# Performance work log

Measured on AMD Instinct MI355X. Metric: run time of the kernel, lower is better.

## Reference

```python
import jax, jax.numpy as jnp
import numpy as np

NEG_INF = -jnp.inf


def setup_inputs() -> dict:
    B, V = 128, 128000
    key = jax.random.key(0)
    k1, k2, k3, k4, k5 = jax.random.split(key, 5)
    logits = jax.random.normal(k1, (B, V), dtype=jnp.float32)
    # temperatures in [0.1, 1.0) to avoid divide-by-tiny blowups
    temperatures = jax.random.uniform(k2, (B,), dtype=jnp.float32) * 0.9 + 0.1
    # min_p typically small, in [0, 0.1)
    min_ps = jax.random.uniform(k3, (B,), dtype=jnp.float32) * 0.1
    # top_p in [0.1, 1.0)
    top_ps = jax.random.uniform(k4, (B,), dtype=jnp.float32) * 0.9 + 0.1
    # top_k in [1, 1000)
    top_ks = jax.random.randint(k5, (B,), 1, 1000, dtype=jnp.int32)
    return {"logits": logits, "temperatures": temperatures, "min_ps": min_ps,
            "top_ps": top_ps, "top_ks": top_ks}


def _apply_top_k_top_p(logits, top_ps, top_ks):
    B, V = logits.shape
    sort_idx = jnp.argsort(logits, axis=-1)  # ascending, matches torch sort(descending=False)
    logits_sort = jnp.take_along_axis(logits, sort_idx, axis=-1)
    # top-k: threshold is the (V-k)-th smallest value; mask anything strictly below it
    thresh_idx = (V - top_ks.astype(jnp.int32))[:, None]          # [B,1]
    thresh = jnp.take_along_axis(logits_sort, thresh_idx, axis=-1)  # [B,1]
    logits_sort = jnp.where(logits_sort < thresh, NEG_INF, logits_sort)
    # top-p: drop smallest tokens whose cumulative prob <= 1 - p; never drop the max token
    probs_sort = jax.nn.softmax(logits_sort, axis=-1)
    probs_sum = jnp.cumsum(probs_sort, axis=-1)
    top_p_mask = probs_sum <= (1.0 - top_ps)[:, None]
    top_p_mask = top_p_mask.at[:, -1].set(False)
    logits_sort = jnp.where(top_p_mask, NEG_INF, logits_sort)
    # scatter back to original vocab order
    rows = jnp.arange(B)[:, None]
    return jnp.zeros_like(logits_sort).at[rows, sort_idx].set(logits_sort)


def _apply_min_p(logits, min_ps):
    probs = jax.nn.softmax(logits, axis=-1)
    top_probs = jnp.max(probs, axis=-1, keepdims=True)
    remove = probs < min_ps[:, None] * top_probs
    return jnp.where(remove, NEG_INF, logits)


def reference(logits, temperatures, min_ps, top_ps, top_ks):
    logits = logits.astype(jnp.float32) / temperatures[:, None]
    logits = _apply_top_k_top_p(logits, top_ps, top_ks)
    logits = _apply_min_p(logits, min_ps)
    # torch.multinomial(softmax(logits), 1) == categorical sampling from logits
    sample_key = jax.random.key(42)
    next_tokens = jax.random.categorical(sample_key, logits, axis=-1)  # [B]
    return next_tokens
```

## Files before the change

### kernel.cpp

```cpp
#include <hip/hip_runtime.h>
#include <stdint.h>

#define HBINS 4096
#define CAND 2048
#define NSLICES 32
#define HTHREADS 256
#define CTHREADS 256
#define STHREADS 1024

typedef unsigned int u32;
typedef unsigned long long u64;

__device__ __forceinline__ u32 f2s(float f) {
  u32 b = __float_as_uint(f);
  return b ^ ((b & 0x80000000u) ? 0xFFFFFFFFu : 0x80000000u);
}
__device__ __forceinline__ float s2f(u32 s) {
  u32 b = (s & 0x80000000u) ? (s ^ 0x80000000u) : ~s;
  return __uint_as_float(b);
}
__device__ __forceinline__ u32 rotl32(u32 x, int r) { return (x << r) | (x >> (32 - r)); }

__device__ __forceinline__ u64 shfl_xor_u64(u64 v, int mask) {
  int lo = __shfl_xor((int)(u32)v, mask, 64);
  int hi = __shfl_xor((int)(u32)(v >> 32), mask, 64);
  return ((u64)(u32)hi << 32) | (u32)lo;
}

__device__ __forceinline__ u32 threefry_bits(u32 ctr) {
  const u32 ks0 = 0u, ks1 = 42u, ks2 = 0x1BD11BDAu ^ 0u ^ 42u;
  u32 x0 = ks0;
  u32 x1 = ctr + ks1;
#define TFR(r) { x0 += x1; x1 = rotl32(x1, (r)); x1 ^= x0; }
  TFR(13) TFR(15) TFR(26) TFR(6)   x0 += ks1; x1 += ks2 + 1u;
  TFR(17) TFR(29) TFR(16) TFR(24)  x0 += ks2; x1 += ks0 + 2u;
  TFR(13) TFR(15) TFR(26) TFR(6)   x0 += ks0; x1 += ks1 + 3u;
  TFR(17) TFR(29) TFR(16) TFR(24)  x0 += ks1; x1 += ks2 + 4u;
  TFR(13) TFR(15) TFR(26) TFR(6)   x0 += ks2; x1 += ks0 + 5u;
#undef TFR
  return x0 ^ x1;
}

__global__ __launch_bounds__(HTHREADS)
void hist_kernel(const float* __restrict__ logits, u32* __restrict__ ghist,
                 int V, int slice_len) {
  const int row = blockIdx.x / NSLICES;
  const int sl  = blockIdx.x % NSLICES;
  const int tid = threadIdx.x;
  __shared__ u32 h[HBINS];
  for (int i = tid; i < HBINS; i += HTHREADS) h[i] = 0u;
  __syncthreads();
  int rem = V - sl * slice_len;
  if (rem > slice_len) rem = slice_len;
  if (rem < 0) rem = 0;
  const float* src = logits + (size_t)row * (size_t)V + (size_t)sl * slice_len;
  const int n4 = rem >> 2;
  const float4* p4 = (const float4*)src;
  for (int i = tid; i < n4; i += HTHREADS) {
    float4 w = p4[i];
    atomicAdd(&h[f2s(w.x) >> 20], 1u);
    atomicAdd(&h[f2s(w.y) >> 20], 1u);
    atomicAdd(&h[f2s(w.z) >> 20], 1u);
    atomicAdd(&h[f2s(w.w) >> 20], 1u);
  }
  for (int i = (n4 << 2) + tid; i < rem; i += HTHREADS)
    atomicAdd(&h[f2s(src[i]) >> 20], 1u);
  __syncthreads();
  u32* gh = ghist + (size_t)row * HBINS;
  for (int i = tid; i < HBINS; i += HTHREADS) {
    u32 c = h[i];
    if (c) atomicAdd(&gh[i], c);
  }
}

__global__ __launch_bounds__(256)
void select_kernel(const u32* __restrict__ ghist, const int* __restrict__ topks,
                   u32* __restrict__ gthr, u32* __restrict__ gcs,
                   u32* __restrict__ gcount, int V) {
  const int row = blockIdx.x;
  const int tid = threadIdx.x;
  __shared__ u32 hist[HBINS];
  __shared__ u32 part[256];
  __shared__ u32 chunk[64];
  const u32* gh = ghist + (size_t)row * HBINS;
  for (int i = tid; i < HBINS; i += 256) hist[i] = gh[i];
  __syncthreads();
  {
    u32 s = 0;
    for (int j = 0; j < 16; ++j) s += hist[tid * 16 + j];
    part[tid] = s;
  }
  __syncthreads();
  if (tid < 64)
    chunk[tid] = part[tid * 4] + part[tid * 4 + 1] + part[tid * 4 + 2] + part[tid * 4 + 3];
  __syncthreads();
  if (tid == 0) {
    int k = topks[row];
    if (k < 1) k = 1;
    if (k > V) k = V;
    const u32 ku = (u32)k;
    u32 acc = 0;
    int cstar = 0;
    for (int c = 63; c >= 0; --c) {
      if (acc + chunk[c] >= ku) { cstar = c; break; }
      acc += chunk[c];
    }
    int pstar = cstar * 4;
    for (int p = cstar * 4 + 3; p >= cstar * 4; --p) {
      if (acc + part[p] >= ku) { pstar = p; break; }
      acc += part[p];
    }
    int bstar = pstar * 16;
    for (int bq = pstar * 16 + 15; bq >= pstar * 16; --bq) {
      acc += hist[bq];
      if (acc >= ku) { bstar = bq; break; }
    }
    gthr[row] = (u32)bstar << 20;
    gcs[row] = (acc < (u32)CAND ? acc : (u32)CAND);
    gcount[row] = 0u;
  }
}

__global__ __launch_bounds__(CTHREADS)
void collect_kernel(const float* __restrict__ logits,
                    const float* __restrict__ temps,
                    const u32* __restrict__ gthr,
                    u32* __restrict__ gcount,
                    u64* __restrict__ gcand, int V, int slice_len) {
  const int row = blockIdx.x / NSLICES;
  const int sl  = blockIdx.x % NSLICES;
  const int tid = threadIdx.x;

  __shared__ u64 stage[CAND];
  __shared__ int sh_cnt, sh_base;
  if (tid == 0) sh_cnt = 0;
  __syncthreads();

  const u32 thr = gthr[row];
  const float t = temps[row];
  int rem = V - sl * slice_len;
  if (rem > slice_len) rem = slice_len;
  if (rem < 0) rem = 0;
  const float* src = logits + (size_t)row * (size_t)V + (size_t)sl * slice_len;
  const u32 ibase = (u32)(sl * slice_len);
  const int n4 = rem >> 2;
  const float4* p4 = (const float4*)src;
  for (int i = tid; i < n4; i += CTHREADS) {
    float4 w = p4[i];
    if (f2s(w.x) >= thr) { int pos = atomicAdd(&sh_cnt, 1); if (pos < CAND) stage[pos] = ((u64)f2s(w.x / t) << 32) | (ibase + 4u * i + 0u); }
    if (f2s(w.y) >= thr) { int pos = atomicAdd(&sh_cnt, 1); if (pos < CAND) stage[pos] = ((u64)f2s(w.y / t) << 32) | (ibase + 4u * i + 1u); }
    if (f2s(w.z) >= thr) { int pos = atomicAdd(&sh_cnt, 1); if (pos < CAND) stage[pos] = ((u64)f2s(w.z / t) << 32) | (ibase + 4u * i + 2u); }
    if (f2s(w.w) >= thr) { int pos = atomicAdd(&sh_cnt, 1); if (pos < CAND) stage[pos] = ((u64)f2s(w.w / t) << 32) | (ibase + 4u * i + 3u); }
  }
  for (int i = (n4 << 2) + tid; i < rem; i += CTHREADS) {
    float l = src[i];
    if (f2s(l) >= thr) { int pos = atomicAdd(&sh_cnt, 1); if (pos < CAND) stage[pos] = ((u64)f2s(l / t) << 32) | (ibase + (u32)i); }
  }
  __syncthreads();
  int n = sh_cnt;
  if (n > CAND) n = CAND;
  if (tid == 0) sh_base = (int)atomicAdd(&gcount[row], (u32)n);
  __syncthreads();
  const int base = sh_base;
  u64* gc = gcand + (size_t)row * CAND;
  for (int i = tid; i < n; i += CTHREADS) {
    int dst = base + i;
    if (dst < CAND) gc[dst] = stage[i];
  }
}

__global__ __launch_bounds__(STHREADS)
void Sampler_73529840107542_kernel(const float* __restrict__ minps,
                                   const float* __restrict__ topps,
                                   const int* __restrict__ topks,
                                   const u32* __restrict__ gcs,
                                   const u64* __restrict__ gcand,
                                   int* __restrict__ out, int V) {
  const int b = blockIdx.x;
  const int tid = threadIdx.x;
  const int w = tid >> 6, l = tid & 63;
  const float one_minus_p = 1.0f - topps[b];
  const float minp = minps[b];
  int k = topks[b];
  if (k < 1) k = 1;
  if (k > V) k = V;

  __shared__ u64 cand[CAND];
  __shared__ u64 scand[CAND];
  __shared__ float eBuf[CAND];
  __shared__ float bufA[CAND];
  __shared__ float bufB[CAND];
  __shared__ unsigned char keepf[CAND];
  __shared__ u32 rbin[256];
  __shared__ float wredf[16];
  __shared__ u64 wred64[16];
  __shared__ int sh_byte, sh_above, sh_ns;
  __shared__ float sh_Z1, sh_Z2;

  const int cs = (int)gcs[b];
  const u64* gc = gcand + (size_t)b * CAND;
  for (int c = tid; c < cs; c += STHREADS) cand[c] = gc[c];
  if (tid == 0) sh_ns = 0;
  __syncthreads();

  u32 prefix = 0u;
  u32 remk = (u32)k;
  for (int pass = 0; pass < 4; ++pass) {
    const int shift = 24 - 8 * pass;
    if (tid < 256) rbin[tid] = 0u;
    __syncthreads();
    const u32 mask = (pass == 0) ? 0u : (0xFFFFFFFFu << (shift + 8));
    for (int c = tid; c < cs; c += STHREADS) {
      u32 s = (u32)(cand[c] >> 32);
      if (((s ^ prefix) & mask) == 0u)
        atomicAdd(&rbin[(s >> shift) & 255u], 1u);
    }
    __syncthreads();
    if (w == 0) {
      u32 b0 = rbin[4 * l], b1 = rbin[4 * l + 1], b2 = rbin[4 * l + 2], b3 = rbin[4 * l + 3];
      u32 q3 = b3, q2 = b2 + q3, q1 = b1 + q2, q0 = b0 + q1;
      u32 inc = q0;
      #pragma unroll
      for (int off = 1; off < 64; off <<= 1) {
        int src = l + off;
        u32 o = (u32)__shfl((int)inc, src < 64 ? src : l, 64);
        inc += (src < 64) ? o : 0u;
      }
      u32 excl = inc - q0;
      u64 ball = __ballot(excl + q0 >= remk);
      int lsel = 63 - __clzll(ball);
      if (l == lsel) {
        int i; u32 above;
        if      (excl + q3 >= remk) { i = 3; above = excl; }
        else if (excl + q2 >= remk) { i = 2; above = excl + q3; }
        else if (excl + q1 >= remk) { i = 1; above = excl + q2; }
        else                        { i = 0; above = excl + q1; }
        sh_byte = 4 * l + i;
        sh_above = (int)above;
      }
    }
    __syncthreads();
    prefix |= ((u32)sh_byte) << shift;
    remk -= (u32)sh_above;
  }
  const u32 Ts = prefix;

  for (int c = tid; c < cs; c += STHREADS) {
    u64 key = cand[c];
    if ((u32)(key >> 32) >= Ts) {
      int pos = atomicAdd(&sh_ns, 1);
      scand[pos] = key;
    }
  }
  __syncthreads();
  const int ns = sh_ns;

  int SN = 128;
  while (SN < ns) SN <<= 1;
  const int NW = SN >> 7;
  const bool act = (w < NW);
  const int e_lo = (w << 7) + l;
  const int e_hi = e_lo + 64;
  const u64 SENT = 0xFFFFFFFFFFFFFFFFull;
  u64 k0 = (act && e_lo < ns) ? scand[e_lo] : SENT;
  u64 k1 = (act && e_hi < ns) ? scand[e_hi] : SENT;
  for (int size = 2; size <= SN; size <<= 1) {
    for (int s = size >> 1; s > 0; s >>= 1) {
      if (s >= 128) {
        if (act) { scand[e_lo] = k0; scand[e_hi] = k1; }
        __syncthreads();
        if (act) {
          u64 p0 = scand[e_lo ^ s], p1 = scand[e_hi ^ s];
          bool km0 = (((e_lo & s) == 0) == ((e_lo & size) == 0));
          if (km0 ? (p0 < k0) : (p0 > k0)) k0 = p0;
          bool km1 = (((e_hi & s) == 0) == ((e_hi & size) == 0));
          if (km1 ? (p1 < k1) : (p1 > k1)) k1 = p1;
        }
        __syncthreads();
      } else if (act) {
        if (s == 64) {
          bool asc = ((e_lo & size) == 0);
          if ((k0 > k1) == asc) { u64 t = k0; k0 = k1; k1 = t; }
        } else {
          u64 p0 = shfl_xor_u64(k0, s);
          u64 p1 = shfl_xor_u64(k1, s);
          bool km0 = (((l & s) == 0) == ((e_lo & size) == 0));
          if (km0 ? (p0 < k0) : (p0 > k0)) k0 = p0;
          bool km1 = (((l & s) == 0) == ((e_hi & size) == 0));
          if (km1 ? (p1 < k1) : (p1 > k1)) k1 = p1;
        }
      }
    }
  }
  if (act) { scand[e_lo] = k0; scand[e_hi] = k1; }
  __syncthreads();

  const float m = s2f((u32)(scand[ns - 1] >> 32));

  for (int c = tid; c < ns; c += STHREADS)
    eBuf[c] = expf(s2f((u32)(scand[c] >> 32)) - m);
  __syncthreads();

  {
    float local = 0.0f;
    for (int c = tid; c < ns; c += STHREADS) local += eBuf[c];
    #pragma unroll
    for (int off = 1; off < 64; off <<= 1) local += __shfl_xor(local, off, 64);
    if (l == 0) wredf[w] = local;
    __syncthreads();
    if (w == 0) {
      float v = (l < 16) ? wredf[l] : 0.0f;
      #pragma unroll
      for (int off = 1; off < 64; off <<= 1) v += __shfl_xor(v, off, 64);
      if (l == 0) sh_Z1 = v;
    }
    __syncthreads();
  }

  const float Z1 = sh_Z1;
  for (int c = tid; c < ns; c += STHREADS) bufA[c] = eBuf[c] / Z1;
  __syncthreads();

  if (w == 0) {
    float carry = 0.0f;
    for (int base = 0; base < ns; base += 64) {
      int c = base + l;
      float v = (c < ns) ? bufA[c] : 0.0f;
      float acc = carry;
      #pragma unroll 16
      for (int j = 0; j < 64; ++j) {
        float t = __shfl(v, j, 64);
        acc += (l >= j) ? t : 0.0f;
      }
      if (c < ns) bufB[c] = acc;
      carry = __shfl(acc, 63, 64);
    }
  }
  __syncthreads();

  for (int c = tid; c < ns; c += STHREADS)
    keepf[c] = (c == ns - 1 || bufB[c] > one_minus_p) ? 1 : 0;
  __syncthreads();

  {
    float local = 0.0f;
    for (int c = tid; c < ns; c += STHREADS)
      if (keepf[c]) local += eBuf[c];
    #pragma unroll
    for (int off = 1; off < 64; off <<= 1) local += __shfl_xor(local, off, 64);
    if (l == 0) wredf[w] = local;
    __syncthreads();
    if (w == 0) {
      float v = (l < 16) ? wredf[l] : 0.0f;
      #pragma unroll
      for (int off = 1; off < 64; off <<= 1) v += __shfl_xor(v, off, 64);
      if (l == 0) sh_Z2 = v;
    }
    __syncthreads();
  }

  {
    const float Z2 = sh_Z2;
    const float rhs = minp * (1.0f / Z2);
    for (int c = tid; c < ns; c += STHREADS)
      if (keepf[c] && (eBuf[c] / Z2 < rhs)) keepf[c] = 0;
  }
  __syncthreads();

  {
    const float TINY = 1.17549435082228750797e-38f;
    u64 best = 0ull;
    for (int c = tid; c < ns; c += STHREADS) {
      if (!keepf[c]) continue;
      u32 s = (u32)(scand[c] >> 32);
      u32 idx = (u32)(scand[c] & 0xFFFFFFFFull);
      float x = s2f(s);
      u32 bits = threefry_bits((u32)b * (u32)V + idx);
      float f = __uint_as_float((bits >> 9) | 0x3f800000u) - 1.0f;
      float u = fmaxf(TINY, f * 1.0f + TINY);
      float g = -logf(-logf(u));
      float sc = g + x;
      u64 key = ((u64)f2s(sc) << 32) | (u64)(0xFFFFFFFFu - idx);
      if (key > best) best = key;
    }
    #pragma unroll
    for (int off = 1; off < 64; off <<= 1) {
      u64 o = shfl_xor_u64(best, off);
      if (o > best) best = o;
    }
    if (l == 0) wred64[w] = best;
    __syncthreads();
    if (w == 0) {
      u64 v = (l < 16) ? wred64[l] : 0ull;
      #pragma unroll
      for (int off = 1; off < 64; off <<= 1) {
        u64 o = shfl_xor_u64(v, off);
        if (o > v) v = o;
      }
      if (l == 0) out[b] = (int)(0xFFFFFFFFu - (u32)(v & 0xFFFFFFFFull));
    }
  }
}

extern "C" void kernel_launch(void* const* d_in, const int* in_sizes, int n_in,
                              void* d_out, int out_size, void* d_ws, size_t ws_size,
                              hipStream_t stream) {
  const float* logits = (const float*)d_in[0];
  const float* temps  = (const float*)d_in[1];
  const float* minps  = (const float*)d_in[2];
  const float* topps  = (const float*)d_in[3];
  const int*   topks  = (const int*)d_in[4];
  const int B = in_sizes[1];
  const int V = in_sizes[0] / B;
  (void)n_in; (void)out_size; (void)ws_size;

  u32* ghist  = (u32*)d_ws;
  u32* gcount = ghist + (size_t)B * HBINS;
  u32* gcs    = gcount + B;
  u32* gthr   = gcs + B;
  u64* gcand  = (u64*)(gthr + B);

  const int slice_len = (((V + NSLICES - 1) / NSLICES) + 3) & ~3;

  hipMemsetAsync(ghist, 0, (size_t)B * HBINS * sizeof(u32), stream);
  hist_kernel<<<dim3(B * NSLICES), dim3(HTHREADS), 0, stream>>>(logits, ghist, V, slice_len);
  select_kernel<<<dim3(B), dim3(256), 0, stream>>>(ghist, topks, gthr, gcs, gcount, V);
  collect_kernel<<<dim3(B * NSLICES), dim3(CTHREADS), 0, stream>>>(
      logits, temps, gthr, gcount, gcand, V, slice_len);
  Sampler_73529840107542_kernel<<<dim3(B), dim3(STHREADS), 0, stream>>>(
      minps, topps, topks, gcs, gcand, (int*)d_out, V);
}
```

Measured before the change: 179.0 us.

## Rewrite sampler as single-wavefront kernel with register bitonic sort

The final sampler kernel drops from 1024 threads to one 64-lane wavefront. Block barriers become block fences, the radix histogram gets four privatized copies to cut atomic contention, and compaction uses ballot/popcount instead of shared atomics. Candidate sets of up to 1024 are sorted in registers with shuffle-based bitonic stages. The histogram pass also gets its own slice count (16) separate from the collect pass, so it launches fewer, larger blocks. The cost is far less parallelism per row in the sampler, and a slow LDS fallback sort when there are more than 1024 candidates.

```diff
diff --git a/kernel.cpp b/kernel.cpp
--- a/kernel.cpp
+++ b/kernel.cpp
@@ -3,10 +3,10 @@
 
 #define HBINS 4096
 #define CAND 2048
-#define NSLICES 32
+#define HSLICES 16
+#define CSLICES 32
 #define HTHREADS 256
 #define CTHREADS 256
-#define STHREADS 1024
 
 typedef unsigned int u32;
 typedef unsigned long long u64;
@@ -41,11 +41,39 @@
   return x0 ^ x1;
 }
 
+template<int SIZE>
+__device__ __forceinline__ void shfl_sweep(u64* keys, int nr, int l) {
+  for (int s = (SIZE / 2 < 32 ? SIZE / 2 : 32); s >= 1; s >>= 1) {
+#pragma unroll
+    for (int r = 0; r < 16; ++r) {
+      if (r < nr) {
+        u64 pk = shfl_xor_u64(keys[r], s);
+        bool asc = ((((r << 6) + l) & SIZE) == 0);
+        bool keepmin = (((l & s) == 0) == asc);
+        if (keepmin ? (pk < keys[r]) : (pk > keys[r])) keys[r] = pk;
+      }
+    }
+  }
+}
+template<int SIZE, int D>
+__device__ __forceinline__ void local_phase(u64* keys, int nr) {
+#pragma unroll
+  for (int r = 0; r < 16; ++r) {
+    if (((r & D) == 0) && ((r | D) < 16)) {
+      if ((r | D) < nr) {
+        bool asc = (((r << 6) & SIZE) == 0);
+        u64 a = keys[r], b2 = keys[r | D];
+        if ((a > b2) == asc) { keys[r] = b2; keys[r | D] = a; }
+      }
+    }
+  }
+}
+
 __global__ __launch_bounds__(HTHREADS)
 void hist_kernel(const float* __restrict__ logits, u32* __restrict__ ghist,
                  int V, int slice_len) {
-  const int row = blockIdx.x / NSLICES;
-  const int sl  = blockIdx.x % NSLICES;
+  const int row = blockIdx.x / HSLICES;
+  const int sl  = blockIdx.x % HSLICES;
   const int tid = threadIdx.x;
   __shared__ u32 h[HBINS];
   for (int i = tid; i < HBINS; i += HTHREADS) h[i] = 0u;
@@ -127,8 +155,8 @@
                     const u32* __restrict__ gthr,
                     u32* __restrict__ gcount,
                     u64* __restrict__ gcand, int V, int slice_len) {
-  const int row = blockIdx.x / NSLICES;
-  const int sl  = blockIdx.x % NSLICES;
+  const int row = blockIdx.x / CSLICES;
+  const int sl  = blockIdx.x % CSLICES;
   const int tid = threadIdx.x;
 
   __shared__ u64 stage[CAND];
@@ -169,7 +197,7 @@
   }
 }
 
-__global__ __launch_bounds__(STHREADS)
+__global__ __launch_bounds__(64)
 void Sampler_73529840107542_kernel(const float* __restrict__ minps,
                                    const float* __restrict__ topps,
                                    const int* __restrict__ topks,
@@ -177,201 +205,172 @@
                                    const u64* __restrict__ gcand,
                                    int* __restrict__ out, int V) {
   const int b = blockIdx.x;
-  const int tid = threadIdx.x;
-  const int w = tid >> 6, l = tid & 63;
+  const int l = threadIdx.x;
   const float one_minus_p = 1.0f - topps[b];
   const float minp = minps[b];
   int k = topks[b];
   if (k < 1) k = 1;
   if (k > V) k = V;
 
-  __shared__ u64 cand[CAND];
-  __shared__ u64 scand[CAND];
-  __shared__ float eBuf[CAND];
-  __shared__ float bufA[CAND];
-  __shared__ float bufB[CAND];
-  __shared__ unsigned char keepf[CAND];
-  __shared__ u32 rbin[256];
-  __shared__ float wredf[16];
-  __shared__ u64 wred64[16];
-  __shared__ int sh_byte, sh_above, sh_ns;
-  __shared__ float sh_Z1, sh_Z2;
+  __shared__ __align__(16) unsigned char arena[36864];
+  u64* ldsCand = (u64*)(arena);
+  float* eArr  = (float*)(arena);
+  unsigned char* keep = arena + 8192;
+  u64* scand   = (u64*)(arena + 16384);
+  u32* rbin    = (u32*)(arena + 32768);
 
   const int cs = (int)gcs[b];
   const u64* gc = gcand + (size_t)b * CAND;
-  for (int c = tid; c < cs; c += STHREADS) cand[c] = gc[c];
-  if (tid == 0) sh_ns = 0;
-  __syncthreads();
+  for (int c = l; c < cs; c += 64) ldsCand[c] = gc[c];
+  __threadfence_block();
 
   u32 prefix = 0u;
   u32 remk = (u32)k;
   for (int pass = 0; pass < 4; ++pass) {
     const int shift = 24 - 8 * pass;
-    if (tid < 256) rbin[tid] = 0u;
-    __syncthreads();
+    for (int i = l; i < 1024; i += 64) rbin[i] = 0u;
+    __threadfence_block();
     const u32 mask = (pass == 0) ? 0u : (0xFFFFFFFFu << (shift + 8));
-    for (int c = tid; c < cs; c += STHREADS) {
-      u32 s = (u32)(cand[c] >> 32);
+    for (int c = l; c < cs; c += 64) {
+      u32 s = (u32)(ldsCand[c] >> 32);
       if (((s ^ prefix) & mask) == 0u)
-        atomicAdd(&rbin[(s >> shift) & 255u], 1u);
-    }
-    __syncthreads();
-    if (w == 0) {
-      u32 b0 = rbin[4 * l], b1 = rbin[4 * l + 1], b2 = rbin[4 * l + 2], b3 = rbin[4 * l + 3];
-      u32 q3 = b3, q2 = b2 + q3, q1 = b1 + q2, q0 = b0 + q1;
-      u32 inc = q0;
-      #pragma unroll
-      for (int off = 1; off < 64; off <<= 1) {
-        int src = l + off;
-        u32 o = (u32)__shfl((int)inc, src < 64 ? src : l, 64);
-        inc += (src < 64) ? o : 0u;
+        atomicAdd(&rbin[((l & 3) << 8) + ((s >> shift) & 255u)], 1u);
+    }
+    __threadfence_block();
+    u32 b0 = rbin[4 * l]     + rbin[256 + 4 * l]     + rbin[512 + 4 * l]     + rbin[768 + 4 * l];
+    u32 b1 = rbin[4 * l + 1] + rbin[256 + 4 * l + 1] + rbin[512 + 4 * l + 1] + rbin[768 + 4 * l + 1];
+    u32 b2 = rbin[4 * l + 2] + rbin[256 + 4 * l + 2] + rbin[512 + 4 * l + 2] + rbin[768 + 4 * l + 2];
+    u32 b3 = rbin[4 * l + 3] + rbin[256 + 4 * l + 3] + rbin[512 + 4 * l + 3] + rbin[768 + 4 * l + 3];
+    u32 q3 = b3, q2 = b2 + q3, q1 = b1 + q2, q0 = b0 + q1;
+    u32 inc = q0;
+#pragma unroll
+    for (int off = 1; off < 64; off <<= 1) {
+      int src = l + off;
+      u32 o = (u32)__shfl((int)inc, src < 64 ? src : l, 64);
+      inc += (src < 64) ? o : 0u;
+    }
+    u32 excl = inc - q0;
+    u64 ball = __ballot(excl + q0 >= remk);
+    int lsel = 63 - __clzll(ball);
+    int ii; u32 above;
+    if      (excl + q3 >= remk) { ii = 3; above = excl; }
+    else if (excl + q2 >= remk) { ii = 2; above = excl + q3; }
+    else if (excl + q1 >= remk) { ii = 1; above = excl + q2; }
+    else                        { ii = 0; above = excl + q1; }
+    u32 mybyte = (u32)(4 * l + ii);
+    u32 selbyte = (u32)__shfl((int)mybyte, lsel, 64);
+    u32 selabove = (u32)__shfl((int)above, lsel, 64);
+    prefix |= selbyte << shift;
+    remk -= selabove;
+  }
+  const u32 Ts = prefix;
+
+  int ns = 0;
+  for (int base2 = 0; base2 < cs; base2 += 64) {
+    int c = base2 + l;
+    u64 key = 0ull;
+    bool pred = false;
+    if (c < cs) {
+      key = ldsCand[c];
+      pred = ((u32)(key >> 32) >= Ts);
+    }
+    u64 ball = __ballot(pred);
+    if (pred) scand[ns + (int)__popcll(ball & ((1ull << l) - 1ull))] = key;
+    ns += (int)__popcll(ball);
+  }
+  __threadfence_block();
+
+  const u64 SENT = 0xFFFFFFFFFFFFFFFFull;
+  if (ns <= 1024) {
+    int SN = 64;
+    while (SN < ns) SN <<= 1;
+    const int nr = SN >> 6;
+    u64 keys[16];
+#pragma unroll
+    for (int r = 0; r < 16; ++r) {
+      if (r < nr) {
+        int e = (r << 6) + l;
+        keys[r] = (e < ns) ? scand[e] : SENT;
       }
-      u32 excl = inc - q0;
-      u64 ball = __ballot(excl + q0 >= remk);
-      int lsel = 63 - __clzll(ball);
-      if (l == lsel) {
-        int i; u32 above;
-        if      (excl + q3 >= remk) { i = 3; above = excl; }
-        else if (excl + q2 >= remk) { i = 2; above = excl + q3; }
-        else if (excl + q1 >= remk) { i = 1; above = excl + q2; }
-        else                        { i = 0; above = excl + q1; }
-        sh_byte = 4 * l + i;
-        sh_above = (int)above;
+    }
+    if (SN >= 2)  shfl_sweep<2>(keys, nr, l);
+    if (SN >= 4)  shfl_sweep<4>(keys, nr, l);
+    if (SN >= 8)  shfl_sweep<8>(keys, nr, l);
+    if (SN >= 16) shfl_sweep<16>(keys, nr, l);
+    if (SN >= 32) shfl_sweep<32>(keys, nr, l);
+    if (SN >= 64) shfl_sweep<64>(keys, nr, l);
+    if (SN >= 128)  { local_phase<128, 1>(keys, nr); shfl_sweep<128>(keys, nr, l); }
+    if (SN >= 256)  { local_phase<256, 2>(keys, nr); local_phase<256, 1>(keys, nr); shfl_sweep<256>(keys, nr, l); }
+    if (SN >= 512)  { local_phase<512, 4>(keys, nr); local_phase<512, 2>(keys, nr); local_phase<512, 1>(keys, nr); shfl_sweep<512>(keys, nr, l); }
+    if (SN >= 1024) { local_phase<1024, 8>(keys, nr); local_phase<1024, 4>(keys, nr); local_phase<1024, 2>(keys, nr); local_phase<1024, 1>(keys, nr); shfl_sweep<1024>(keys, nr, l); }
+#pragma unroll
+    for (int r = 0; r < 16; ++r)
+      if (r < nr) scand[(r << 6) + l] = keys[r];
+  } else {
+    for (int c = ns + l; c < CAND; c += 64) scand[c] = SENT;
+    __threadfence_block();
+    for (int size = 2; size <= CAND; size <<= 1) {
+      for (int s = size >> 1; s > 0; s >>= 1) {
+        for (int i = l; i < CAND; i += 64) {
+          int j = i ^ s;
+          if (j > i) {
+            u64 a = scand[i], b2 = scand[j];
+            bool asc = ((i & size) == 0);
+            if ((a > b2) == asc) { scand[i] = b2; scand[j] = a; }
+          }
+        }
+        __threadfence_block();
       }
     }
-    __syncthreads();
-    prefix |= ((u32)sh_byte) << shift;
-    remk -= (u32)sh_above;
-  }
-  const u32 Ts = prefix;
-
-  for (int c = tid; c < cs; c += STHREADS) {
-    u64 key = cand[c];
-    if ((u32)(key >> 32) >= Ts) {
-      int pos = atomicAdd(&sh_ns, 1);
-      scand[pos] = key;
-    }
-  }
-  __syncthreads();
-  const int ns = sh_ns;
-
-  int SN = 128;
-  while (SN < ns) SN <<= 1;
-  const int NW = SN >> 7;
-  const bool act = (w < NW);
-  const int e_lo = (w << 7) + l;
-  const int e_hi = e_lo + 64;
-  const u64 SENT = 0xFFFFFFFFFFFFFFFFull;
-  u64 k0 = (act && e_lo < ns) ? scand[e_lo] : SENT;
-  u64 k1 = (act && e_hi < ns) ? scand[e_hi] : SENT;
-  for (int size = 2; size <= SN; size <<= 1) {
-    for (int s = size >> 1; s > 0; s >>= 1) {
-      if (s >= 128) {
-        if (act) { scand[e_lo] = k0; scand[e_hi] = k1; }
-        __syncthreads();
-        if (act) {
-          u64 p0 = scand[e_lo ^ s], p1 = scand[e_hi ^ s];
-          bool km0 = (((e_lo & s) == 0) == ((e_lo & size) == 0));
-          if (km0 ? (p0 < k0) : (p0 > k0)) k0 = p0;
-          bool km1 = (((e_hi & s) == 0) == ((e_hi & size) == 0));
-          if (km1 ? (p1 < k1) : (p1 > k1)) k1 = p1;
-        }
-        __syncthreads();
-      } else if (act) {
-        if (s == 64) {
-          bool asc = ((e_lo & size) == 0);
-          if ((k0 > k1) == asc) { u64 t = k0; k0 = k1; k1 = t; }
-        } else {
-          u64 p0 = shfl_xor_u64(k0, s);
-          u64 p1 = shfl_xor_u64(k1, s);
-          bool km0 = (((l & s) == 0) == ((e_lo & size) == 0));
-          if (km0 ? (p0 < k0) : (p0 > k0)) k0 = p0;
-          bool km1 = (((l & s) == 0) == ((e_hi & size) == 0));
-          if (km1 ? (p1 < k1) : (p1 > k1)) k1 = p1;
-        }
-      }
-    }
-  }
-  if (act) { scand[e_lo] = k0; scand[e_hi] = k1; }
-  __syncthreads();
+  }
+  __threadfence_block();
 
   const float m = s2f((u32)(scand[ns - 1] >> 32));
 
-  for (int c = tid; c < ns; c += STHREADS)
-    eBuf[c] = expf(s2f((u32)(scand[c] >> 32)) - m);
-  __syncthreads();
+  for (int c = l; c < ns; c += 64)
+    eArr[c] = expf(s2f((u32)(scand[c] >> 32)) - m);
+
+  float z1l = 0.0f;
+  for (int c = l; c < ns; c += 64) z1l += eArr[c];
+#pragma unroll
+  for (int off = 1; off < 64; off <<= 1) z1l += __shfl_xor(z1l, off, 64);
+  const float Z1 = z1l;
 
   {
-    float local = 0.0f;
-    for (int c = tid; c < ns; c += STHREADS) local += eBuf[c];
-    #pragma unroll
-    for (int off = 1; off < 64; off <<= 1) local += __shfl_xor(local, off, 64);
-    if (l == 0) wredf[w] = local;
-    __syncthreads();
-    if (w == 0) {
-      float v = (l < 16) ? wredf[l] : 0.0f;
-      #pragma unroll
-      for (int off = 1; off < 64; off <<= 1) v += __shfl_xor(v, off, 64);
-      if (l == 0) sh_Z1 = v;
-    }
-    __syncthreads();
-  }
-
-  const float Z1 = sh_Z1;
-  for (int c = tid; c < ns; c += STHREADS) bufA[c] = eBuf[c] / Z1;
-  __syncthreads();
-
-  if (w == 0) {
     float carry = 0.0f;
-    for (int base = 0; base < ns; base += 64) {
-      int c = base + l;
-      float v = (c < ns) ? bufA[c] : 0.0f;
+    for (int base2 = 0; base2 < ns; base2 += 64) {
+      int c = base2 + l;
+      float v = (c < ns) ? (eArr[c] / Z1) : 0.0f;
       float acc = carry;
-      #pragma unroll 16
+#pragma unroll 16
       for (int j = 0; j < 64; ++j) {
         float t = __shfl(v, j, 64);
         acc += (l >= j) ? t : 0.0f;
       }
-      if (c < ns) bufB[c] = acc;
+      if (c < ns)
+        keep[c] = (c == ns - 1 || acc > one_minus_p) ? 1 : 0;
       carry = __shfl(acc, 63, 64);
     }
   }
-  __syncthreads();
-
-  for (int c = tid; c < ns; c += STHREADS)
-    keepf[c] = (c == ns - 1 || bufB[c] > one_minus_p) ? 1 : 0;
-  __syncthreads();
+
+  float z2l = 0.0f;
+  for (int c = l; c < ns; c += 64)
+    if (keep[c]) z2l += eArr[c];
+#pragma unroll
+  for (int off = 1; off < 64; off <<= 1) z2l += __shfl_xor(z2l, off, 64);
+  const float Z2 = z2l;
 
   {
-    float local = 0.0f;
-    for (int c = tid; c < ns; c += STHREADS)
-      if (keepf[c]) local += eBuf[c];
-    #pragma unroll
-    for (int off = 1; off < 64; off <<= 1) local += __shfl_xor(local, off, 64);
-    if (l == 0) wredf[w] = local;
-    __syncthreads();
-    if (w == 0) {
-      float v = (l < 16) ? wredf[l] : 0.0f;
-      #pragma unroll
-      for (int off = 1; off < 64; off <<= 1) v += __shfl_xor(v, off, 64);
-      if (l == 0) sh_Z2 = v;
-    }
-    __syncthreads();
-  }
-
-  {
-    const float Z2 = sh_Z2;
     const float rhs = minp * (1.0f / Z2);
-    for (int c = tid; c < ns; c += STHREADS)
-      if (keepf[c] && (eBuf[c] / Z2 < rhs)) keepf[c] = 0;
-  }
-  __syncthreads();
+    for (int c = l; c < ns; c += 64)
+      if (keep[c] && (eArr[c] / Z2 < rhs)) keep[c] = 0;
+  }
 
   {
     const float TINY = 1.17549435082228750797e-38f;
     u64 best = 0ull;
-    for (int c = tid; c < ns; c += STHREADS) {
-      if (!keepf[c]) continue;
+    for (int c = l; c < ns; c += 64) {
+      if (!keep[c]) continue;
       u32 s = (u32)(scand[c] >> 32);
       u32 idx = (u32)(scand[c] & 0xFFFFFFFFull);
       float x = s2f(s);
@@ -383,22 +382,12 @@
       u64 key = ((u64)f2s(sc) << 32) | (u64)(0xFFFFFFFFu - idx);
       if (key > best) best = key;
     }
-    #pragma unroll
+#pragma unroll
     for (int off = 1; off < 64; off <<= 1) {
       u64 o = shfl_xor_u64(best, off);
       if (o > best) best = o;
     }
-    if (l == 0) wred64[w] = best;
-    __syncthreads();
-    if (w == 0) {
-      u64 v = (l < 16) ? wred64[l] : 0ull;
-      #pragma unroll
-      for (int off = 1; off < 64; off <<= 1) {
-        u64 o = shfl_xor_u64(v, off);
-        if (o > v) v = o;
-      }
-      if (l == 0) out[b] = (int)(0xFFFFFFFFu - (u32)(v & 0xFFFFFFFFull));
-    }
+    if (l == 0) out[b] = (int)(0xFFFFFFFFu - (u32)(best & 0xFFFFFFFFull));
   }
 }
 
@@ -420,13 +409,14 @@
   u32* gthr   = gcs + B;
   u64* gcand  = (u64*)(gthr + B);
 
-  const int slice_len = (((V + NSLICES - 1) / NSLICES) + 3) & ~3;
+  const int hslice = (((V + HSLICES - 1) / HSLICES) + 3) & ~3;
+  const int cslice = (((V + CSLICES - 1) / CSLICES) + 3) & ~3;
 
   hipMemsetAsync(ghist, 0, (size_t)B * HBINS * sizeof(u32), stream);
-  hist_kernel<<<dim3(B * NSLICES), dim3(HTHREADS), 0, stream>>>(logits, ghist, V, slice_len);
+  hist_kernel<<<dim3(B * HSLICES), dim3(HTHREADS), 0, stream>>>(logits, ghist, V, hslice);
   select_kernel<<<dim3(B), dim3(256), 0, stream>>>(ghist, topks, gthr, gcs, gcount, V);
-  collect_kernel<<<dim3(B * NSLICES), dim3(CTHREADS), 0, stream>>>(
-      logits, temps, gthr, gcount, gcand, V, slice_len);
-  Sampler_73529840107542_kernel<<<dim3(B), dim3(STHREADS), 0, stream>>>(
+  collect_kernel<<<dim3(B * CSLICES), dim3(CTHREADS), 0, stream>>>(
+      logits, temps, gthr, gcount, gcand, V, cslice);
+  Sampler_73529840107542_kernel<<<dim3(B), dim3(64), 0, stream>>>(
       minps, topps, topks, gcs, gcand, (int*)d_out, V);
 }
```

Measured after the change: 256.1 us. +43.1%, slower.

## Fuse histogram, threshold select and candidate collection into one per-slice kernel

Applied to the files above, without the earlier changes.

Replaces the global histogram, per-row select kernel and collect kernel with a single kernel in which each slice builds a local histogram, picks a local threshold keeping roughly its top 128 values, and writes those candidates. This removes the large ghist memset, two launches and one of the two passes over the logits from global memory. The sampler also switches to warp-aggregated ballot atomics for its radix histogram, merges several shared buffers into one arena, and fuses the cumsum with the keep-flag step. The risk is correctness for top_k near 1000: 16 slices times 128 local candidates gives only about 2048 per row, so a slice holding many true top-k values could drop some of them.

```diff
diff --git a/kernel.cpp b/kernel.cpp
--- a/kernel.cpp
+++ b/kernel.cpp
@@ -2,11 +2,13 @@
 #include <stdint.h>
 
 #define HBINS 4096
-#define CAND 2048
-#define NSLICES 32
-#define HTHREADS 256
+#define CAND 4096
+#define SCAP 2048
+#define CSLICES 16
 #define CTHREADS 256
 #define STHREADS 1024
+#define TLOC 128
+#define STAGECAP 1024
 
 typedef unsigned int u32;
 typedef unsigned long long u64;
@@ -41,50 +43,42 @@
   return x0 ^ x1;
 }
 
-__global__ __launch_bounds__(HTHREADS)
-void hist_kernel(const float* __restrict__ logits, u32* __restrict__ ghist,
-                 int V, int slice_len) {
-  const int row = blockIdx.x / NSLICES;
-  const int sl  = blockIdx.x % NSLICES;
+__global__ __launch_bounds__(CTHREADS)
+void collect2_kernel(const float* __restrict__ logits,
+                     const float* __restrict__ temps,
+                     u32* __restrict__ gcount,
+                     u64* __restrict__ gcand, int V, int slice_len) {
+  const int row = blockIdx.x / CSLICES;
+  const int sl  = blockIdx.x % CSLICES;
   const int tid = threadIdx.x;
-  __shared__ u32 h[HBINS];
-  for (int i = tid; i < HBINS; i += HTHREADS) h[i] = 0u;
-  __syncthreads();
+
+  __shared__ u32 hist[HBINS];
+  __shared__ u64 stage[STAGECAP];
+  __shared__ u32 part[CTHREADS];
+  __shared__ u32 chunkv[64];
+  __shared__ int sh_thr, sh_cnt, sh_base;
+
+  for (int i = tid; i < HBINS; i += CTHREADS) hist[i] = 0u;
+  __syncthreads();
+
   int rem = V - sl * slice_len;
   if (rem > slice_len) rem = slice_len;
   if (rem < 0) rem = 0;
   const float* src = logits + (size_t)row * (size_t)V + (size_t)sl * slice_len;
   const int n4 = rem >> 2;
   const float4* p4 = (const float4*)src;
-  for (int i = tid; i < n4; i += HTHREADS) {
+
+  for (int i = tid; i < n4; i += CTHREADS) {
     float4 w = p4[i];
-    atomicAdd(&h[f2s(w.x) >> 20], 1u);
-    atomicAdd(&h[f2s(w.y) >> 20], 1u);
-    atomicAdd(&h[f2s(w.z) >> 20], 1u);
-    atomicAdd(&h[f2s(w.w) >> 20], 1u);
-  }
-  for (int i = (n4 << 2) + tid; i < rem; i += HTHREADS)
-    atomicAdd(&h[f2s(src[i]) >> 20], 1u);
-  __syncthreads();
-  u32* gh = ghist + (size_t)row * HBINS;
-  for (int i = tid; i < HBINS; i += HTHREADS) {
-    u32 c = h[i];
-    if (c) atomicAdd(&gh[i], c);
-  }
-}
-
-__global__ __launch_bounds__(256)
-void select_kernel(const u32* __restrict__ ghist, const int* __restrict__ topks,
-                   u32* __restrict__ gthr, u32* __restrict__ gcs,
-                   u32* __restrict__ gcount, int V) {
-  const int row = blockIdx.x;
-  const int tid = threadIdx.x;
-  __shared__ u32 hist[HBINS];
-  __shared__ u32 part[256];
-  __shared__ u32 chunk[64];
-  const u32* gh = ghist + (size_t)row * HBINS;
-  for (int i = tid; i < HBINS; i += 256) hist[i] = gh[i];
-  __syncthreads();
+    atomicAdd(&hist[f2s(w.x) >> 20], 1u);
+    atomicAdd(&hist[f2s(w.y) >> 20], 1u);
+    atomicAdd(&hist[f2s(w.z) >> 20], 1u);
+    atomicAdd(&hist[f2s(w.w) >> 20], 1u);
+  }
+  for (int i = (n4 << 2) + tid; i < rem; i += CTHREADS)
+    atomicAdd(&hist[f2s(src[i]) >> 20], 1u);
+  __syncthreads();
+
   {
     u32 s = 0;
     for (int j = 0; j < 16; ++j) s += hist[tid * 16 + j];
@@ -92,18 +86,15 @@
   }
   __syncthreads();
   if (tid < 64)
-    chunk[tid] = part[tid * 4] + part[tid * 4 + 1] + part[tid * 4 + 2] + part[tid * 4 + 3];
+    chunkv[tid] = part[tid * 4] + part[tid * 4 + 1] + part[tid * 4 + 2] + part[tid * 4 + 3];
   __syncthreads();
   if (tid == 0) {
-    int k = topks[row];
-    if (k < 1) k = 1;
-    if (k > V) k = V;
-    const u32 ku = (u32)k;
+    u32 ku = (u32)((rem < TLOC) ? (rem > 0 ? rem : 1) : TLOC);
     u32 acc = 0;
     int cstar = 0;
     for (int c = 63; c >= 0; --c) {
-      if (acc + chunk[c] >= ku) { cstar = c; break; }
-      acc += chunk[c];
+      if (acc + chunkv[c] >= ku) { cstar = c; break; }
+      acc += chunkv[c];
     }
     int pstar = cstar * 4;
     for (int p = cstar * 4 + 3; p >= cstar * 4; --p) {
@@ -115,50 +106,28 @@
       acc += hist[bq];
       if (acc >= ku) { bstar = bq; break; }
     }
-    gthr[row] = (u32)bstar << 20;
-    gcs[row] = (acc < (u32)CAND ? acc : (u32)CAND);
-    gcount[row] = 0u;
-  }
-}
-
-__global__ __launch_bounds__(CTHREADS)
-void collect_kernel(const float* __restrict__ logits,
-                    const float* __restrict__ temps,
-                    const u32* __restrict__ gthr,
-                    u32* __restrict__ gcount,
-                    u64* __restrict__ gcand, int V, int slice_len) {
-  const int row = blockIdx.x / NSLICES;
-  const int sl  = blockIdx.x % NSLICES;
-  const int tid = threadIdx.x;
-
-  __shared__ u64 stage[CAND];
-  __shared__ int sh_cnt, sh_base;
-  if (tid == 0) sh_cnt = 0;
-  __syncthreads();
-
-  const u32 thr = gthr[row];
+    sh_thr = (int)(((u32)bstar) << 20);
+    sh_cnt = 0;
+  }
+  __syncthreads();
+
+  const u32 thr = (u32)sh_thr;
   const float t = temps[row];
-  int rem = V - sl * slice_len;
-  if (rem > slice_len) rem = slice_len;
-  if (rem < 0) rem = 0;
-  const float* src = logits + (size_t)row * (size_t)V + (size_t)sl * slice_len;
   const u32 ibase = (u32)(sl * slice_len);
-  const int n4 = rem >> 2;
-  const float4* p4 = (const float4*)src;
   for (int i = tid; i < n4; i += CTHREADS) {
     float4 w = p4[i];
-    if (f2s(w.x) >= thr) { int pos = atomicAdd(&sh_cnt, 1); if (pos < CAND) stage[pos] = ((u64)f2s(w.x / t) << 32) | (ibase + 4u * i + 0u); }
-    if (f2s(w.y) >= thr) { int pos = atomicAdd(&sh_cnt, 1); if (pos < CAND) stage[pos] = ((u64)f2s(w.y / t) << 32) | (ibase + 4u * i + 1u); }
-    if (f2s(w.z) >= thr) { int pos = atomicAdd(&sh_cnt, 1); if (pos < CAND) stage[pos] = ((u64)f2s(w.z / t) << 32) | (ibase + 4u * i + 2u); }
-    if (f2s(w.w) >= thr) { int pos = atomicAdd(&sh_cnt, 1); if (pos < CAND) stage[pos] = ((u64)f2s(w.w / t) << 32) | (ibase + 4u * i + 3u); }
+    if (f2s(w.x) >= thr) { int pos = atomicAdd(&sh_cnt, 1); if (pos < STAGECAP) stage[pos] = ((u64)f2s(w.x / t) << 32) | (ibase + 4u * i + 0u); }
+    if (f2s(w.y) >= thr) { int pos = atomicAdd(&sh_cnt, 1); if (pos < STAGECAP) stage[pos] = ((u64)f2s(w.y / t) << 32) | (ibase + 4u * i + 1u); }
+    if (f2s(w.z) >= thr) { int pos = atomicAdd(&sh_cnt, 1); if (pos < STAGECAP) stage[pos] = ((u64)f2s(w.z / t) << 32) | (ibase + 4u * i + 2u); }
+    if (f2s(w.w) >= thr) { int pos = atomicAdd(&sh_cnt, 1); if (pos < STAGECAP) stage[pos] = ((u64)f2s(w.w / t) << 32) | (ibase + 4u * i + 3u); }
   }
   for (int i = (n4 << 2) + tid; i < rem; i += CTHREADS) {
-    float l = src[i];
-    if (f2s(l) >= thr) { int pos = atomicAdd(&sh_cnt, 1); if (pos < CAND) stage[pos] = ((u64)f2s(l / t) << 32) | (ibase + (u32)i); }
+    float lg = src[i];
+    if (f2s(lg) >= thr) { int pos = atomicAdd(&sh_cnt, 1); if (pos < STAGECAP) stage[pos] = ((u64)f2s(lg / t) << 32) | (ibase + (u32)i); }
   }
   __syncthreads();
   int n = sh_cnt;
-  if (n > CAND) n = CAND;
+  if (n > STAGECAP) n = STAGECAP;
   if (tid == 0) sh_base = (int)atomicAdd(&gcount[row], (u32)n);
   __syncthreads();
   const int base = sh_base;
@@ -173,7 +142,7 @@
 void Sampler_73529840107542_kernel(const float* __restrict__ minps,
                                    const float* __restrict__ topps,
                                    const int* __restrict__ topks,
-                                   const u32* __restrict__ gcs,
+                                   const u32* __restrict__ gcount,
                                    const u64* __restrict__ gcand,
                                    int* __restrict__ out, int V) {
   const int b = blockIdx.x;
@@ -185,19 +154,19 @@
   if (k < 1) k = 1;
   if (k > V) k = V;
 
-  __shared__ u64 cand[CAND];
-  __shared__ u64 scand[CAND];
-  __shared__ float eBuf[CAND];
-  __shared__ float bufA[CAND];
-  __shared__ float bufB[CAND];
-  __shared__ unsigned char keepf[CAND];
-  __shared__ u32 rbin[256];
+  __shared__ __align__(16) unsigned char arena[50176];
+  u64* cand   = (u64*)(arena);
+  float* eBuf = (float*)(arena);
+  unsigned char* keepf = arena + 8192;
+  u64* scand  = (u64*)(arena + 32768);
+  u32* rbin   = (u32*)(arena + 49152);
   __shared__ float wredf[16];
   __shared__ u64 wred64[16];
   __shared__ int sh_byte, sh_above, sh_ns;
   __shared__ float sh_Z1, sh_Z2;
 
-  const int cs = (int)gcs[b];
+  int cs = (int)gcount[b];
+  if (cs > CAND) cs = CAND;
   const u64* gc = gcand + (size_t)b * CAND;
   for (int c = tid; c < cs; c += STHREADS) cand[c] = gc[c];
   if (tid == 0) sh_ns = 0;
@@ -210,17 +179,30 @@
     if (tid < 256) rbin[tid] = 0u;
     __syncthreads();
     const u32 mask = (pass == 0) ? 0u : (0xFFFFFFFFu << (shift + 8));
-    for (int c = tid; c < cs; c += STHREADS) {
-      u32 s = (u32)(cand[c] >> 32);
-      if (((s ^ prefix) & mask) == 0u)
-        atomicAdd(&rbin[(s >> shift) & 255u], 1u);
+    const int iters = (cs + STHREADS - 1) / STHREADS;
+    for (int it = 0; it < iters; ++it) {
+      int c = it * STHREADS + tid;
+      bool active = false;
+      u32 bin = 0;
+      if (c < cs) {
+        u32 s = (u32)(cand[c] >> 32);
+        if (((s ^ prefix) & mask) == 0u) { active = true; bin = (s >> shift) & 255u; }
+      }
+      u64 ball = __ballot(active);
+      while (ball) {
+        int leader = __ffsll((unsigned long long)ball) - 1;
+        u32 lbin = (u32)__shfl((int)bin, leader, 64);
+        u64 same = __ballot(active && bin == lbin);
+        if (l == leader) atomicAdd(&rbin[lbin], (u32)__popcll(same));
+        ball &= ~same;
+      }
     }
     __syncthreads();
     if (w == 0) {
       u32 b0 = rbin[4 * l], b1 = rbin[4 * l + 1], b2 = rbin[4 * l + 2], b3 = rbin[4 * l + 3];
       u32 q3 = b3, q2 = b2 + q3, q1 = b1 + q2, q0 = b0 + q1;
       u32 inc = q0;
-      #pragma unroll
+#pragma unroll
       for (int off = 1; off < 64; off <<= 1) {
         int src = l + off;
         u32 o = (u32)__shfl((int)inc, src < 64 ? src : l, 64);
@@ -249,11 +231,12 @@
     u64 key = cand[c];
     if ((u32)(key >> 32) >= Ts) {
       int pos = atomicAdd(&sh_ns, 1);
-      scand[pos] = key;
-    }
-  }
-  __syncthreads();
-  const int ns = sh_ns;
+      if (pos < SCAP) scand[pos] = key;
+    }
+  }
+  __syncthreads();
+  int ns = sh_ns;
+  if (ns > SCAP) ns = SCAP;
 
   int SN = 128;
   while (SN < ns) SN <<= 1;
@@ -304,55 +287,49 @@
   {
     float local = 0.0f;
     for (int c = tid; c < ns; c += STHREADS) local += eBuf[c];
-    #pragma unroll
+#pragma unroll
     for (int off = 1; off < 64; off <<= 1) local += __shfl_xor(local, off, 64);
     if (l == 0) wredf[w] = local;
     __syncthreads();
     if (w == 0) {
       float v = (l < 16) ? wredf[l] : 0.0f;
-      #pragma unroll
+#pragma unroll
       for (int off = 1; off < 64; off <<= 1) v += __shfl_xor(v, off, 64);
       if (l == 0) sh_Z1 = v;
     }
     __syncthreads();
   }
-
   const float Z1 = sh_Z1;
-  for (int c = tid; c < ns; c += STHREADS) bufA[c] = eBuf[c] / Z1;
-  __syncthreads();
 
   if (w == 0) {
     float carry = 0.0f;
-    for (int base = 0; base < ns; base += 64) {
-      int c = base + l;
-      float v = (c < ns) ? bufA[c] : 0.0f;
+    for (int base2 = 0; base2 < ns; base2 += 64) {
+      int c = base2 + l;
+      float v = (c < ns) ? (eBuf[c] / Z1) : 0.0f;
       float acc = carry;
-      #pragma unroll 16
+#pragma unroll 16
       for (int j = 0; j < 64; ++j) {
         float t = __shfl(v, j, 64);
         acc += (l >= j) ? t : 0.0f;
       }
-      if (c < ns) bufB[c] = acc;
+      if (c < ns)
+        keepf[c] = (c == ns - 1 || acc > one_minus_p) ? 1 : 0;
       carry = __shfl(acc, 63, 64);
     }
   }
-  __syncthreads();
-
-  for (int c = tid; c < ns; c += STHREADS)
-    keepf[c] = (c == ns - 1 || bufB[c] > one_minus_p) ? 1 : 0;
   __syncthreads();
 
   {
     float local = 0.0f;
     for (int c = tid; c < ns; c += STHREADS)
       if (keepf[c]) local += eBuf[c];
-    #pragma unroll
+#pragma unroll
     for (int off = 1; off < 64; off <<= 1) local += __shfl_xor(local, off, 64);
     if (l == 0) wredf[w] = local;
     __syncthreads();
     if (w == 0) {
       float v = (l < 16) ? wredf[l] : 0.0f;
-      #pragma unroll
+#pragma unroll
       for (int off = 1; off < 64; off <<= 1) v += __shfl_xor(v, off, 64);
       if (l == 0) sh_Z2 = v;
     }
@@ -383,7 +360,7 @@
       u64 key = ((u64)f2s(sc) << 32) | (u64)(0xFFFFFFFFu - idx);
       if (key > best) best = key;
     }
-    #pragma unroll
+#pragma unroll
     for (int off = 1; off < 64; off <<= 1) {
       u64 o = shfl_xor_u64(best, off);
       if (o > best) best = o;
@@ -392,7 +369,7 @@
     __syncthreads();
     if (w == 0) {
       u64 v = (l < 16) ? wred64[l] : 0ull;
-      #pragma unroll
+#pragma unroll
       for (int off = 1; off < 64; off <<= 1) {
         u64 o = shfl_xor_u64(v, off);
         if (o > v) v = o;
@@ -414,19 +391,14 @@
   const int V = in_sizes[0] / B;
   (void)n_in; (void)out_size; (void)ws_size;
 
-  u32* ghist  = (u32*)d_ws;
-  u32* gcount = ghist + (size_t)B * HBINS;
-  u32* gcs    = gcount + B;
-  u32* gthr   = gcs + B;
-  u64* gcand  = (u64*)(gthr + B);
-
-  const int slice_len = (((V + NSLICES - 1) / NSLICES) + 3) & ~3;
-
-  hipMemsetAsync(ghist, 0, (size_t)B * HBINS * sizeof(u32), stream);
-  hist_kernel<<<dim3(B * NSLICES), dim3(HTHREADS), 0, stream>>>(logits, ghist, V, slice_len);
-  select_kernel<<<dim3(B), dim3(256), 0, stream>>>(ghist, topks, gthr, gcs, gcount, V);
-  collect_kernel<<<dim3(B * NSLICES), dim3(CTHREADS), 0, stream>>>(
-      logits, temps, gthr, gcount, gcand, V, slice_len);
+  u32* gcount = (u32*)d_ws;
+  u64* gcand  = (u64*)((char*)d_ws + ((B * 4 + 511) & ~511));
+
+  const int slice_len = (((V + CSLICES - 1) / CSLICES) + 3) & ~3;
+
+  hipMemsetAsync(gcount, 0, (size_t)B * sizeof(u32), stream);
+  collect2_kernel<<<dim3(B * CSLICES), dim3(CTHREADS), 0, stream>>>(
+      logits, temps, gcount, gcand, V, slice_len);
   Sampler_73529840107542_kernel<<<dim3(B), dim3(STHREADS), 0, stream>>>(
-      minps, topps, topks, gcs, gcand, (int*)d_out, V);
-}
+      minps, topps, topks, gcount, gcand, (int*)d_out, V);
+}
```

Result: no change. 180.3 us (+0.7%).
